# Performance work log

Measured on AMD Instinct MI355X. Metric: run time of the kernel, lower is better.

The kernel has to match this reference:

```python
import jax, jax.numpy as jnp
from jax import lax
import numpy as np

B, EMB, HEADS, LAYERS = 32, 512, 8, 4
SEQ_JD, TOK = 200, 50

def _mask_lg(S):
    # Faithful vectorization of CoKEModel.mask_lg (True = masked)
    m = np.ones((B, HEADS, S, S), dtype=bool)
    rows = np.arange(S)[:, None]
    cols = np.clip(rows - 5 + np.arange(10)[None, :], 0, S - 1)  # window=10, offset -5..4
    for h in range(6):  # local_len = 6 local-window heads
        m[:, h, rows, cols] = False
    m[0, 6:] = False          # global heads unmasked only for batch 0 (faithful to source)
    m[:, :, 0, :] = False     # CLS row attends everywhere
    return m

def _ln_free(x):
    # CoKEModel.layer_norm: no affine, eps=1e-12, rsqrt form
    mu = jnp.mean(x, axis=-1, keepdims=True)
    sx = x - mu
    v = jnp.mean(sx * sx, axis=-1, keepdims=True)
    return sx * jnp.sqrt(1.0 / (v + 1e-12))

def _ln(x, g, b):
    mu = jnp.mean(x, axis=-1, keepdims=True)
    sx = x - mu
    v = jnp.mean(sx * sx, axis=-1, keepdims=True)
    return sx / jnp.sqrt(v + 1e-5) * g + b

def _textcnn(tokens, emb, cws, cbs, fw, fb):
    e = emb[tokens]                        # (N, 50, 1024)
    x = jnp.transpose(e, (0, 2, 1))        # (N, 1024, 50): embed dim as channels
    pooled = []
    for W, b in zip(cws, cbs):             # W: (100, k, 1024)
        rhs = jnp.transpose(W, (0, 2, 1))  # (100, 1024, k)
        y = lax.conv_general_dilated(x, rhs, (1,), 'VALID', dimension_numbers=('NCH', 'OIH', 'NCH'))
        y = jax.nn.relu(y + b[None, :, None])
        pooled.append(jnp.max(y, axis=2))  # global max-pool over time
    return jnp.concatenate(pooled, axis=1) @ fw.T + fb   # (N, 512)

def _encoder(x, mask, wq, bq, wk, bk, wv, bv, wo, bo, l1g, l1b, fw1, fb1, fw2, fb2, l2g, l2b):
    Bb, S, D = x.shape
    dh = D // HEADS
    scale = 1.0 / (dh ** 0.5)
    for l in range(LAYERS):
        q = (x @ wq[l].T + bq[l]).reshape(Bb, S, HEADS, dh)
        k = (x @ wk[l].T + bk[l]).reshape(Bb, S, HEADS, dh)
        v = (x @ wv[l].T + bv[l]).reshape(Bb, S, HEADS, dh)
        s = jnp.einsum('bshd,bthd->bhst', q, k) * scale
        s = jnp.where(mask, -1e9, s)
        a = jax.nn.softmax(s, axis=-1)
        c = jnp.einsum('bhst,bthd->bshd', a, v).reshape(Bb, S, D)
        x = _ln(x + c @ wo[l].T + bo[l], l1g[l], l1b[l])
        h = jax.nn.relu(x @ fw1[l].T + fb1[l])
        x = _ln(x + h @ fw2[l].T + fb2[l], l2g[l], l2b[l])
    return x

def _contrastive(im, s, margin=0.02):
    sc = im @ s.T
    d = jnp.diag(sc)
    cs = jnp.maximum(margin + sc - d[:, None], 0.0)
    ci = jnp.maximum(margin + sc - d[None, :], 0.0)
    eye = jnp.eye(sc.shape[0], dtype=bool)
    cs = jnp.where(eye, 0.0, cs)
    ci = jnp.where(eye, 0.0, ci)
    return jnp.sum(cs) + jnp.sum(ci)

def _forward(floats, src, mask101, mask200):
    (user_info, label_similarity, emb_tc, cw1, cb1, cw2, cb2, cw3, cb3, tfw, tfb,
     wq, bq, wk, bk, wv, bv, wo, bo, l1g, l1b, fw1, fb1, fw2, fb2, l2g, l2b,
     fc1w, fc1b, fc2w, fc2b, fc3w, fc3b, fc4w, fc4b, pscale, pbias) = floats
    cws, cbs = (cw1, cw2, cw3), (cb1, cb2, cb3)
    enc = (wq, bq, wk, bk, wv, bv, wo, bo, l1g, l1b, fw1, fb1, fw2, fb2, l2g, l2b)

    # ---- first pass: first 100 JDs + global CLS token ----
    s1 = _textcnn(src[:, :100].reshape(-1, TOK), emb_tc, cws, cbs, tfw, tfb).reshape(B, 100, EMB)
    s1 = _ln_free(s1)
    s1 = jnp.concatenate([jnp.zeros((B, 1, EMB), s1.dtype), s1], axis=1)  # (B, 101, EMB)
    p = _encoder(s1, mask101, *enc)
    p = jax.nn.gelu(p @ fc1w.T + fc1b, approximate=False)
    p = _ln_free(p)
    p = p * pscale[:, :p.shape[1]] + pbias[:, :p.shape[1]]
    p = p @ fc2w.T + fc2b                      # (B, 101, 204)
    cls_e, tok = p[:, :1], p[:, 1:]
    P = tok @ fc3w.T + fc3b                    # (B, 100, 204)
    clsIII = cls_e @ fc3w.T + fc3b             # (B, 1, 204)
    SLl = jnp.einsum('bsm,bsn->bmn', P, P)     # P^T @ P
    SL_hat = label_similarity[None] + 0.4 * SLl
    outIII = jnp.squeeze(clsIII @ SL_hat, axis=1)  # (B, 204)

    # ---- second pass: all 200 JDs ----
    s2 = _textcnn(src.reshape(-1, TOK), emb_tc, cws, cbs, tfw, tfb).reshape(B, SEQ_JD, EMB)
    s2 = _ln_free(s2)
    ap = _encoder(s2, mask200, *enc)
    ap = jax.nn.gelu(ap @ fc1w.T + fc1b, approximate=False)
    ap = _ln_free(ap)
    ap = ap * pscale[:, :SEQ_JD] + pbias[:, :SEQ_JD]
    p1 = ap @ fc2w.T + fc2b                    # (B, 200, 204)

    nn_ = SEQ_JD // 100  # = 2 neighbors
    eps = 1e-6
    skl_rows, seuc_rows = [], []
    for i in range(nn_):
        # NOTE: faithful to source slicing bug: [i : (i+1)*100]
        c1 = jax.nn.softmax(jnp.mean(p1[:, i:(i + 1) * 100], axis=1), axis=-1)
        a1 = jax.nn.softmax(jnp.mean(ap[:, i:(i + 1) * 100], axis=1), axis=-1)
        rk, re = [], []
        for j in range(nn_):
            c2 = jax.nn.softmax(jnp.mean(p1[:, j:(j + 1) * 100], axis=1), axis=-1)
            a2 = jax.nn.softmax(jnp.mean(ap[:, j:(j + 1) * 100], axis=1), axis=-1)
            rk.append(jnp.sum((c1 + eps) * jnp.log((c1 + eps) / (c2 + eps)), axis=-1))
            re.append(jnp.sqrt(jnp.sum((a1 - a2) ** 2, axis=-1) + 1e-12))
        skl_rows.append(jnp.stack(rk, axis=-1))
        seuc_rows.append(jnp.stack(re, axis=-1))
    skl = jnp.stack(skl_rows, axis=1).reshape(B, -1) * 10.0
    seuc = jnp.stack(seuc_rows, axis=1).reshape(B, -1)
    skl = jax.nn.softmax(skl, axis=-1)
    seuc = jax.nn.softmax(seuc, axis=-1)
    loss_sims = jnp.mean(jnp.sum((skl + eps) * jnp.log((skl + eps) / (seuc + eps)), axis=-1))

    cls4m = jnp.squeeze(cls_e, axis=1)
    user4m = user_info @ fc4w.T + fc4b
    nrm = lambda x: x / jnp.maximum(jnp.linalg.norm(x, axis=1, keepdims=True), 1e-12)
    match = _contrastive(nrm(cls4m), nrm(user4m))

    return (jax.nn.softmax(outIII, axis=-1),
            jax.nn.softmax(cls_e, axis=-1),
            loss_sims * 100000.0,
            match * 0.01)

def setup_inputs():
    key = jax.random.key(0)
    kit = iter(jax.random.split(key, 48))
    def nrm(shape, s=0.02):
        return jax.random.normal(next(kit), shape, jnp.float32) * s
    d = {}
    d['src'] = jax.random.randint(next(kit), (B, SEQ_JD, TOK), 0, 20000)
    d['user_info'] = nrm((B, 142), 1.0)
    d['label_similarity'] = nrm((204, 204))
    d['emb_tc'] = nrm((20000, 1024)).at[0].set(0.0)  # padding_idx=0 row zeroed
    d['cw1'], d['cb1'] = nrm((100, 1, 1024)), jnp.zeros((100,), jnp.float32)
    d['cw2'], d['cb2'] = nrm((100, 2, 1024)), jnp.zeros((100,), jnp.float32)
    d['cw3'], d['cb3'] = nrm((100, 3, 1024)), jnp.zeros((100,), jnp.float32)
    d['tfw'], d['tfb'] = nrm((512, 300)), jnp.zeros((512,), jnp.float32)
    d['wq'], d['bq'] = nrm((LAYERS, EMB, EMB)), jnp.zeros((LAYERS, EMB), jnp.float32)
    d['wk'], d['bk'] = nrm((LAYERS, EMB, EMB)), jnp.zeros((LAYERS, EMB), jnp.float32)
    d['wv'], d['bv'] = nrm((LAYERS, EMB, EMB)), jnp.zeros((LAYERS, EMB), jnp.float32)
    d['wo'], d['bo'] = nrm((LAYERS, EMB, EMB)), jnp.zeros((LAYERS, EMB), jnp.float32)
    d['l1g'], d['l1b'] = jnp.ones((LAYERS, EMB), jnp.float32), jnp.zeros((LAYERS, EMB), jnp.float32)
    d['fw1'], d['fb1'] = nrm((LAYERS, 2048, EMB)), jnp.zeros((LAYERS, 2048), jnp.float32)
    d['fw2'], d['fb2'] = nrm((LAYERS, EMB, 2048)), jnp.zeros((LAYERS, EMB), jnp.float32)
    d['l2g'], d['l2b'] = jnp.ones((LAYERS, EMB), jnp.float32), jnp.zeros((LAYERS, EMB), jnp.float32)
    d['fc1w'], d['fc1b'] = nrm((EMB, EMB)), jnp.zeros((EMB,), jnp.float32)
    d['fc2w'], d['fc2b'] = nrm((204, EMB)), jnp.zeros((204,), jnp.float32)
    d['fc3w'], d['fc3b'] = nrm((204, 204)), jnp.zeros((204,), jnp.float32)
    d['fc4w'], d['fc4b'] = nrm((204, 142)), jnp.zeros((204,), jnp.float32)
    d['pscale'] = jnp.ones((B, 300, EMB), jnp.float32)
    d['pbias'] = jnp.zeros((B, 300, EMB), jnp.float32)
    d['mask101'] = jnp.asarray(_mask_lg(101))
    d['mask200'] = jnp.asarray(_mask_lg(SEQ_JD))
    return d

def reference(src, user_info, label_similarity, emb_tc, cw1, cb1, cw2, cb2, cw3, cb3, tfw, tfb, wq, bq, wk, bk, wv, bv, wo, bo, l1g, l1b, fw1, fb1, fw2, fb2, l2g, l2b, fc1w, fc1b, fc2w, fc2b, fc3w, fc3b, fc4w, fc4b, pscale, pbias, mask101, mask200):
    floats = (user_info, label_similarity, emb_tc, cw1, cb1, cw2, cb2, cw3, cb3, tfw, tfb,
              wq, bq, wk, bk, wv, bv, wo, bo, l1g, l1b, fw1, fb1, fw2, fb2, l2g, l2b,
              fc1w, fc1b, fc2w, fc2b, fc3w, fc3b, fc4w, fc4b, pscale, pbias)
    return _forward(floats, src, mask101, mask200)
```

## Files before the change

kernel.cpp:

```cpp
#include <hip/hip_runtime.h>
#include <math.h>

#define EMB 512
#define HEADS 8
#define NLAYERS 4
#define NB 32
#define SEQ 200
#define TOKN 50
#define DH 64
#define FFND 2048
#define NCLS 204
#define VC 640
#define KD 1024
#define CCH 8
#define CROWS (6400/CCH)
#define CM (CROWS*TOKN)
#define MSEG 16
#define CMT ((CM + 127) / 128)
#define CNT (VC / 128)
#define CT  (CMT * CNT)

typedef __attribute__((ext_vector_type(8))) short v8s;
typedef __attribute__((ext_vector_type(4))) float v4f;
typedef unsigned short ushort_t;
// ... 79 lines not shown
    ll[e] = f2bu(x[e] - hf);
  }
  h.x=hh[0]; h.y=hh[1]; h.z=hh[2]; h.w=hh[3];
  l.x=ll[0]; l.y=ll[1]; l.z=ll[2]; l.w=ll[3];
  *(ushort4*)(hi + i4) = h;
  *(ushort4*)(lo + i4) = l;
}

__global__ void qkvbias_kernel(const float* __restrict__ bq, const float* __restrict__ bk,
                               const float* __restrict__ bv, float* __restrict__ bqkv){
  int l = blockIdx.x;
  for (int j = threadIdx.x; j < 1536; j += 256){
    float v;
    if (j < 512) v = bq[l * 512 + j];
    else if (j < 1024) v = bk[l * 512 + j - 512];
    else v = bv[l * 512 + j - 1024];
    bqkv[l * 1536 + j] = v;
  }
}

__global__ __launch_bounds__(256) void zerobuf_kernel(float* __restrict__ p, size_t n4){
  size_t i = (size_t)blockIdx.x * 256 + threadIdx.x;
  size_t stride = (size_t)gridDim.x * 256;
  for (; i < n4; i += stride)
    ((float4*)p)[i] = make_float4(0.f, 0.f, 0.f, 0.f);
}

__global__ __launch_bounds__(256, 4) void conv_gemm_kernel(
    const int* __restrict__ tok, const ushort_t* __restrict__ embb,
    const ushort_t* __restrict__ Wb, ushort_t* __restrict__ Cout, int Mc)
{
  __shared__ ushort_t Al[128][40];
  __shared__ ushort_t Bl[128][40];
  const int tid = threadIdx.x;
  const int t = xcd_swz(blockIdx.x, CT);
  const int n0 = (t % CNT) * 128;
  const int m0 = (t / CNT) * 128;
  const int wave = tid >> 6, lane = tid & 63;
  const int wm = (wave >> 1) * 64, wn = (wave & 1) * 64;
  const int lcol = lane & 15, lq = lane >> 4;

  v4f acc[4][4];
  #pragma unroll
  for (int i = 0; i < 4; i++)
    #pragma unroll
    for (int j = 0; j < 4; j++) acc[i][j] = (v4f){0.f, 0.f, 0.f, 0.f};

  const int srow = tid >> 1, skh = (tid & 1) * 16;
  const int am = m0 + srow;
  const ushort_t* aep = (am < Mc) ? (embb + (size_t)tok[am] * KD + skh) : nullptr;
  const ushort_t* bep = Wb + (size_t)(n0 + srow) * KD + skh;

  for (int k0 = 0; k0 < KD; k0 += 32){
    uint4 a0 = make_uint4(0,0,0,0), a1 = make_uint4(0,0,0,0);
    if (aep){
      a0 = *(const uint4*)(aep + k0);
      a1 = *(const uint4*)(aep + k0 + 8);
    }
    *(uint4*)&Al[srow][skh]     = a0;
    *(uint4*)&Al[srow][skh + 8] = a1;
    uint4 b0 = *(const uint4*)(bep + k0);
    uint4 b1 = *(const uint4*)(bep + k0 + 8);
    *(uint4*)&Bl[srow][skh]     = b0;
    *(uint4*)&Bl[srow][skh + 8] = b1;
    __syncthreads();

    v8s af[4];
    #pragma unroll
    for (int mi = 0; mi < 4; mi++)
      af[mi] = *(const v8s*)&Al[wm + mi*16 + lcol][lq*8];
    #pragma unroll
    for (int ni = 0; ni < 4; ni++){
      v8s bf = *(const v8s*)&Bl[wn + ni*16 + lcol][lq*8];
      #pragma unroll
      for (int mi = 0; mi < 4; mi++)
        acc[mi][ni] = __builtin_amdgcn_mfma_f32_16x16x32_bf16(af[mi], bf, acc[mi][ni], 0, 0, 0);
    }
    __syncthreads();
  }

  #pragma unroll
  for (int ni = 0; ni < 4; ni++){
    int n = n0 + wn + ni*16 + lcol;
    #pragma unroll
    for (int mi = 0; mi < 4; mi++){
      int mbase = m0 + wm + mi*16 + lq*4;
      #pragma unroll
      for (int rg = 0; rg < 4; rg++){
        int m = mbase + rg;
        if (m < Mc) Cout[(size_t)m * VC + n] = f2bu(acc[mi][ni][rg]);
      }
    }
  }
}

__global__ __launch_bounds__(256, 2) void pool_fc_kernel(
    const ushort_t* __restrict__ Cc, const float* __restrict__ tfwT,
    const float* __restrict__ cb1, const float* __restrict__ cb2,
    const float* __restrict__ cb3, const float* __restrict__ tfb,
    float* __restrict__ basep)
{
  __shared__ ushort_t Sg[VC][54];
  __shared__ float pooled[304];
  __shared__ float red[8];
  const int tid = threadIdx.x;
  const int r = blockIdx.x;

  const unsigned* cr = (const unsigned*)(Cc + (size_t)r * TOKN * VC);
  for (int p = 0; p < TOKN; p++){
    for (int t = tid; t < VC/2; t += 256){
      unsigned u = cr[p * (VC/2) + t];
      Sg[2*t][p]   = (ushort_t)(u & 0xFFFFu);
      Sg[2*t+1][p] = (ushort_t)(u >> 16);
    }
  }
  __syncthreads();

  for (int c = tid; c < 300; c += 256){
    float mv = -1e30f;
    if (c < 100){
      float bb = cb1[c];
      for (int p = 0; p < 50; p++) mv = fmaxf(mv, bu2f(Sg[c][p]) + bb);
    } else if (c < 200){
      int o = c - 100; float bb = cb2[o];
      for (int p = 0; p < 49; p++)
        mv = fmaxf(mv, bu2f(Sg[100 + o][p]) + bu2f(Sg[200 + o][p + 1]) + bb);
    } else {
      int o = c - 200; float bb = cb3[o];
      for (int p = 0; p < 48; p++)
        mv = fmaxf(mv, bu2f(Sg[300 + o][p]) + bu2f(Sg[400 + o][p + 1]) + bu2f(Sg[500 + o][p + 2]) + bb);
    }
    pooled[c] = fmaxf(mv, 0.f);
  }
  __syncthreads();

  float v0 = tfb[tid], v1 = tfb[tid + 256];
  for (int j = 0; j < 300; j++){
    float pj = pooled[j];
    v0 = fmaf(pj, tfwT[(size_t)j * EMB + tid], v0);
    v1 = fmaf(pj, tfwT[(size_t)j * EMB + tid + 256], v1);
  }
  float tot = block_reduce(v0 + v1, red, 4, false);
  float mu = tot * (1.f / 512.f);
  float s0 = v0 - mu, s1 = v1 - mu;
  float var = block_reduce(s0 * s0 + s1 * s1, red, 4, false) * (1.f / 512.f);
  float sc = sqrtf(1.f / (var + 1e-12f));
  basep[(size_t)r * EMB + tid] = s0 * sc;
  basep[(size_t)r * EMB + tid + 256] = s1 * sc;
}

__global__ __launch_bounds__(256, 3) void gemm_mfma_pre_kernel(
    const float* __restrict__ A, const ushort_t* __restrict__ Whi,
    const ushort_t* __restrict__ Wlo, const float* __restrict__ bias,
    float* __restrict__ C, int M, int N, int K, int ldc, int act, int mt, int nt)
{
  __shared__ ushort_t Ahi[128][40];
  __shared__ ushort_t Alo[128][40];
  __shared__ ushort_t Bhi[128][40];
  __shared__ ushort_t Blo[128][40];

  const int tid = threadIdx.x;
  const int t = xcd_swz(blockIdx.x, mt * nt);
  const int n0 = (t % nt) * 128, m0 = (t / nt) * 128;
  const int wave = tid >> 6, lane = tid & 63;
  const int wm = (wave >> 1) * 64, wn = (wave & 1) * 64;
  const int lcol = lane & 15, lq = lane >> 4;

  v4f acc[4][4];
  #pragma unroll
  for (int i = 0; i < 4; i++)
    #pragma unroll
    for (int j = 0; j < 4; j++) acc[i][j] = (v4f){0.f, 0.f, 0.f, 0.f};

  const int srow = tid >> 1;
  const int skh  = (tid & 1) * 16;
  const int am = m0 + srow, bn = n0 + srow;
  const bool mok = (am < M), nok = (bn < N);
  const float* ap = A + (size_t)am * K + skh;
  const ushort_t* bph = Whi + (size_t)bn * K + skh;
  const ushort_t* bpl = Wlo + (size_t)bn * K + skh;

  for (int k0 = 0; k0 < K; k0 += 32){
    bool kfull = (k0 + 32 <= K);
    {
      float av[16];
      if (mok && kfull){
        #pragma unroll
        for (int q = 0; q < 4; q++){
          float4 f = *(const float4*)(ap + k0 + q*4);
          av[q*4+0]=f.x; av[q*4+1]=f.y; av[q*4+2]=f.z; av[q*4+3]=f.w;
        }
      } else {
        #pragma unroll
        for (int e = 0; e < 16; e++){
          int k = k0 + skh + e;
          av[e] = (mok && k < K) ? ap[k0 + e] : 0.f;
        }
      }
      uint4 uh[2], ul[2];
      #pragma unroll
      for (int h = 0; h < 2; h++){
        unsigned hw[8], lw[8];
        #pragma unroll
        for (int e = 0; e < 8; e++){
          float x = av[h*8+e];
          unsigned u = __float_as_uint(x);
          float hf = __uint_as_float(u & 0xFFFF0000u);
          hw[e] = u >> 16;
          lw[e] = f2bu(x - hf);
        }
        uh[h] = make_uint4(hw[0]|(hw[1]<<16), hw[2]|(hw[3]<<16), hw[4]|(hw[5]<<16), hw[6]|(hw[7]<<16));
        ul[h] = make_uint4(lw[0]|(lw[1]<<16), lw[2]|(lw[3]<<16), lw[4]|(lw[5]<<16), lw[6]|(lw[7]<<16));
      }
      *(uint4*)&Ahi[srow][skh]     = uh[0];
      *(uint4*)&Ahi[srow][skh + 8] = uh[1];
      *(uint4*)&Alo[srow][skh]     = ul[0];
      *(uint4*)&Alo[srow][skh + 8] = ul[1];
    }
    {
      uint4 h0 = make_uint4(0,0,0,0), h1 = h0, l0 = h0, l1 = h0;
      if (nok && kfull){
        h0 = *(const uint4*)(bph + k0);
        h1 = *(const uint4*)(bph + k0 + 8);
        l0 = *(const uint4*)(bpl + k0);
        l1 = *(const uint4*)(bpl + k0 + 8);
      } else if (nok){
        ushort_t he[16], le[16];
        #pragma unroll
        for (int e = 0; e < 16; e++){
          int k = k0 + skh + e;
          he[e] = (k < K) ? bph[k0 + e] : (ushort_t)0;
          le[e] = (k < K) ? bpl[k0 + e] : (ushort_t)0;
        }
        h0 = *(uint4*)&he[0]; h1 = *(uint4*)&he[8];
        l0 = *(uint4*)&le[0]; l1 = *(uint4*)&le[8];
      }
      *(uint4*)&Bhi[srow][skh]     = h0;
      *(uint4*)&Bhi[srow][skh + 8] = h1;
      *(uint4*)&Blo[srow][skh]     = l0;
      *(uint4*)&Blo[srow][skh + 8] = l1;
    }
    __syncthreads();

    v8s ah[4], al[4];
    #pragma unroll
    for (int mi = 0; mi < 4; mi++){
      ah[mi] = *(const v8s*)&Ahi[wm + mi*16 + lcol][lq*8];
      al[mi] = *(const v8s*)&Alo[wm + mi*16 + lcol][lq*8];
    }
    #pragma unroll
    for (int ni = 0; ni < 4; ni++){
      v8s bh = *(const v8s*)&Bhi[wn + ni*16 + lcol][lq*8];
      v8s bl = *(const v8s*)&Blo[wn + ni*16 + lcol][lq*8];
      #pragma unroll
      for (int mi = 0; mi < 4; mi++){
        acc[mi][ni] = __builtin_amdgcn_mfma_f32_16x16x32_bf16(ah[mi], bh, acc[mi][ni], 0, 0, 0);
        acc[mi][ni] = __builtin_amdgcn_mfma_f32_16x16x32_bf16(al[mi], bh, acc[mi][ni], 0, 0, 0);
        acc[mi][ni] = __builtin_amdgcn_mfma_f32_16x16x32_bf16(ah[mi], bl, acc[mi][ni], 0, 0, 0);
      }
    }
    __syncthreads();
  }

  #pragma unroll
  for (int ni = 0; ni < 4; ni++){
    int n = n0 + wn + ni*16 + lcol;
    if (n >= N) continue;
    float bv = bias[n];
    #pragma unroll
    for (int mi = 0; mi < 4; mi++){
      int mbase = m0 + wm + mi*16 + lq*4;
      #pragma unroll
      for (int rg = 0; rg < 4; rg++){
        int m = mbase + rg;
        if (m >= M) continue;
        float v = acc[mi][ni][rg] + bv;
        if (act == 1) v = fmaxf(v, 0.f);
        else if (act == 2) v = 0.5f * v * (1.f + erff(v * 0.70710678118654752f));
        C[(size_t)m * ldc + n] = v;
      }
    }
  }
}

__global__ __launch_bounds__(256, 4) void gemm_mfma_pre64_kernel(
    const float* __restrict__ A, const ushort_t* __restrict__ Whi,
    const ushort_t* __restrict__ Wlo, const float* __restrict__ bias,
    float* __restrict__ C, int M, int N, int K, int ldc, int act, int mt, int nt, int ks)
{
  __shared__ ushort_t Ahi[128][40];
  __shared__ ushort_t Alo[128][40];
  __shared__ ushort_t Bhi[64][40];
  __shared__ ushort_t Blo[64][40];

  const int tid = threadIdx.x;
  const int tiles = mt * nt;
  const int t_ = xcd_swz(blockIdx.x, tiles * ks);
  const int slice = t_ / tiles;
  const int t = t_ % tiles;
  const int n0 = (t % nt) * 64, m0 = (t / nt) * 128;
  const int kstep = ((K + 31) / 32 + ks - 1) / ks;
  const int kb = slice * kstep * 32;
  const int ke = min(K, kb + kstep * 32);
  if (kb >= ke) return;
  const int wave = tid >> 6, lane = tid & 63;
  const int wm = (wave >> 1) * 64, wn = (wave & 1) * 32;
  const int lcol = lane & 15, lq = lane >> 4;

  v4f acc[4][2];
  #pragma unroll
  for (int i = 0; i < 4; i++)
    #pragma unroll
    for (int j = 0; j < 2; j++) acc[i][j] = (v4f){0.f, 0.f, 0.f, 0.f};

  const int srow = tid >> 1;
  const int skh  = (tid & 1) * 16;
  const int am = m0 + srow;
  const bool mok = (am < M);
  const float* ap = A + (size_t)am * K + skh;
  const int brow = tid >> 2;
  const int bkq  = (tid & 3) * 8;
  const int bn = n0 + brow;
  const bool nok = (bn < N);
  const ushort_t* bph = Whi + (size_t)bn * K + bkq;
  const ushort_t* bpl = Wlo + (size_t)bn * K + bkq;

  for (int k0 = kb; k0 < ke; k0 += 32){
    bool kfull = (k0 + 32 <= K);
    {
      float av[16];
      if (mok && kfull){
        #pragma unroll
        for (int q = 0; q < 4; q++){
          float4 f = *(const float4*)(ap + k0 + q*4);
          av[q*4+0]=f.x; av[q*4+1]=f.y; av[q*4+2]=f.z; av[q*4+3]=f.w;
        }
      } else {
        #pragma unroll
        for (int e = 0; e < 16; e++){
          int k = k0 + skh + e;
          av[e] = (mok && k < K) ? ap[k0 + e] : 0.f;
        }
      }
      uint4 uh[2], ul[2];
      #pragma unroll
      for (int h = 0; h < 2; h++){
        unsigned hw[8], lw[8];
        #pragma unroll
        for (int e = 0; e < 8; e++){
          float x = av[h*8+e];
          unsigned u = __float_as_uint(x);
          float hf = __uint_as_float(u & 0xFFFF0000u);
          hw[e] = u >> 16;
          lw[e] = f2bu(x - hf);
        }
        uh[h] = make_uint4(hw[0]|(hw[1]<<16), hw[2]|(hw[3]<<16), hw[4]|(hw[5]<<16), hw[6]|(hw[7]<<16));
        ul[h] = make_uint4(lw[0]|(lw[1]<<16), lw[2]|(lw[3]<<16), lw[4]|(lw[5]<<16), lw[6]|(lw[7]<<16));
      }
      *(uint4*)&Ahi[srow][skh]     = uh[0];
      *(uint4*)&Ahi[srow][skh + 8] = uh[1];
      *(uint4*)&Alo[srow][skh]     = ul[0];
      *(uint4*)&Alo[srow][skh + 8] = ul[1];
    }
    {
      uint4 h0 = make_uint4(0,0,0,0), l0 = h0;
      if (nok && kfull){
        h0 = *(const uint4*)(bph + k0);
        l0 = *(const uint4*)(bpl + k0);
      } else if (nok){
        ushort_t he[8], le[8];
        #pragma unroll
        for (int e = 0; e < 8; e++){
          int k = k0 + bkq + e;
          he[e] = (k < K) ? bph[k0 + e] : (ushort_t)0;
          le[e] = (k < K) ? bpl[k0 + e] : (ushort_t)0;
        }
        h0 = *(uint4*)&he[0];
        l0 = *(uint4*)&le[0];
      }
      *(uint4*)&Bhi[brow][bkq] = h0;
      *(uint4*)&Blo[brow][bkq] = l0;
    }
    __syncthreads();

    v8s ah[4], al[4];
    #pragma unroll
    for (int mi = 0; mi < 4; mi++){
      ah[mi] = *(const v8s*)&Ahi[wm + mi*16 + lcol][lq*8];
      al[mi] = *(const v8s*)&Alo[wm + mi*16 + lcol][lq*8];
    }
    #pragma unroll
    for (int ni = 0; ni < 2; ni++){
      v8s bh = *(const v8s*)&Bhi[wn + ni*16 + lcol][lq*8];
      v8s bl = *(const v8s*)&Blo[wn + ni*16 + lcol][lq*8];
      #pragma unroll
      for (int mi = 0; mi < 4; mi++){
        acc[mi][ni] = __builtin_amdgcn_mfma_f32_16x16x32_bf16(ah[mi], bh, acc[mi][ni], 0, 0, 0);
        acc[mi][ni] = __builtin_amdgcn_mfma_f32_16x16x32_bf16(al[mi], bh, acc[mi][ni], 0, 0, 0);
        acc[mi][ni] = __builtin_amdgcn_mfma_f32_16x16x32_bf16(ah[mi], bl, acc[mi][ni], 0, 0, 0);
      }
    }
    __syncthreads();
  }

  #pragma unroll
  for (int ni = 0; ni < 2; ni++){
    int n = n0 + wn + ni*16 + lcol;
    if (n >= N) continue;
    float bv = (ks == 1 || slice == 0) ? bias[n] : 0.f;
    #pragma unroll
    for (int mi = 0; mi < 4; mi++){
      int mbase = m0 + wm + mi*16 + lq*4;
      #pragma unroll
      for (int rg = 0; rg < 4; rg++){
        int m = mbase + rg;
        if (m >= M) continue;
        float v = acc[mi][ni][rg] + bv;
        if (ks == 1){
          if (act == 1) v = fmaxf(v, 0.f);
          else if (act == 2) v = 0.5f * v * (1.f + erff(v * 0.70710678118654752f));
          C[(size_t)m * ldc + n] = v;
        } else {
          atomicAdd(&C[(size_t)m * ldc + n], v);
        }
      }
    }
  }
}

__global__ __launch_bounds__(256, 2) void gemm_mfma_kernel(
    const float* __restrict__ A, const float* __restrict__ W,
    const float* __restrict__ bias, float* __restrict__ C,
// ... 444 lines not shown
    const float* __restrict__ p1, const float* __restrict__ ap,
    float* __restrict__ part)
{
  const int blk = blockIdx.x;
  const int bi = blk / MSEG, seg = blk % MSEG;
  const int b = bi >> 1, i = bi & 1;
  const int start = i;
  const int cnt = (i == 0) ? 100 : 199;
  const int per = (cnt + MSEG - 1) / MSEG;
  const int r0 = seg * per;
  const int r1 = min(r0 + per, cnt);
  float* dst = part + (size_t)blk * 720;
  for (int c = threadIdx.x; c < NCLS + EMB; c += 256){
    float s = 0.f;
    if (c < NCLS){
      for (int rr = r0; rr < r1; rr++)
        s += p1[((size_t)(b * SEQ + start + rr)) * NCLS + c];
    } else {
      int cc = c - NCLS;
      for (int rr = r0; rr < r1; rr++)
        s += ap[((size_t)(b * SEQ + start + rr)) * EMB + cc];
    }
    dst[c] = s;
  }
}

__global__ __launch_bounds__(256) void means_final_kernel(
    const float* __restrict__ part, float* __restrict__ mp, float* __restrict__ ma)
{
  const int bi = blockIdx.x;
  const int i = bi & 1;
  const float icnt = (i == 0) ? (1.f / 100.f) : (1.f / 199.f);
  for (int c = threadIdx.x; c < NCLS + EMB; c += 256){
    float s = 0.f;
    #pragma unroll
    for (int g = 0; g < MSEG; g++)
      s += part[((size_t)(bi * MSEG + g)) * 720 + c];
    if (c < NCLS) mp[(size_t)bi * NCLS + c] = s * icnt;
    else          ma[(size_t)bi * EMB + (c - NCLS)] = s * icnt;
  }
}

__global__ __launch_bounds__(64) void klfinal_kernel(
    const float* __restrict__ cbuf, const float* __restrict__ abuf, float* __restrict__ acc)
{
  const int b = blockIdx.x, lane = threadIdx.x;
  float rk[4], re[4];
  #pragma unroll
  for (int pr = 0; pr < 4; pr++){
    int i = pr >> 1, j = pr & 1;
    const float* c1 = cbuf + ((size_t)(b * 2 + i)) * NCLS;
    const float* c2 = cbuf + ((size_t)(b * 2 + j)) * NCLS;
    float s = 0.f;
    for (int n = lane; n < NCLS; n += 64){
      float x = c1[n] + 1e-6f, y = c2[n] + 1e-6f;
      s += x * logf(x / y);
    }
    #pragma unroll
    for (int o = 32; o > 0; o >>= 1) s += __shfl_down(s, o, 64);
    rk[pr] = __shfl(s, 0, 64);
    const float* a1 = abuf + ((size_t)(b * 2 + i)) * EMB;
    const float* a2 = abuf + ((size_t)(b * 2 + j)) * EMB;
    float s2 = 0.f;
    for (int n = lane; n < EMB; n += 64){
      float dd = a1[n] - a2[n];
      s2 += dd * dd;
    }
    #pragma unroll
    for (int o = 32; o > 0; o >>= 1) s2 += __shfl_down(s2, o, 64);
    re[pr] = sqrtf(__shfl(s2, 0, 64) + 1e-12f);
  }
  if (lane == 0){
    float sk[4], se[4];
    float mk = -INFINITY, me = -INFINITY;
    for (int p = 0; p < 4; p++){
      sk[p] = rk[p] * 10.f;
      mk = fmaxf(mk, sk[p]);
      se[p] = re[p];
      me = fmaxf(me, se[p]);
    }
    float ssk = 0.f, sse = 0.f;
    for (int p = 0; p < 4; p++){ sk[p] = expf(sk[p] - mk); ssk += sk[p]; se[p] = expf(se[p] - me); sse += se[p]; }
    float loss = 0.f;
    for (int p = 0; p < 4; p++){
      float x = sk[p] / ssk + 1e-6f, y = se[p] / sse + 1e-6f;
      loss += x * logf(x / y);
    }
    atomicAdd(acc, loss);
  }
}

__global__ void finalize_kernel(const float* __restrict__ acc, float* __restrict__ out){
  if (threadIdx.x == 0) out[13056] = acc[0] * (100000.f / 32.f);
}

extern "C" void kernel_launch(void* const* d_in, const int* in_sizes, int n_in,
                              void* d_out, int out_size, void* d_ws, size_t ws_size,
                              hipStream_t stream)
{
  (void)in_sizes; (void)n_in; (void)out_size;
  const int*   src  = (const int*)  d_in[0];
  const float* user_info = (const float*)d_in[1];
  const float* ls   = (const float*)d_in[2];
  const float* emb  = (const float*)d_in[3];
  const float* cw1  = (const float*)d_in[4];  const float* cb1 = (const float*)d_in[5];
  const float* cw2  = (const float*)d_in[6];  const float* cb2 = (const float*)d_in[7];
  const float* cw3  = (const float*)d_in[8];  const float* cb3 = (const float*)d_in[9];
  const float* tfw  = (const float*)d_in[10]; const float* tfb = (const float*)d_in[11];
  const float* wq   = (const float*)d_in[12]; const float* bq  = (const float*)d_in[13];
  const float* wk   = (const float*)d_in[14]; const float* bk  = (const float*)d_in[15];
  const float* wv   = (const float*)d_in[16]; const float* bv  = (const float*)d_in[17];
  const float* wo   = (const float*)d_in[18]; const float* bo  = (const float*)d_in[19];
  const float* l1g  = (const float*)d_in[20]; const float* l1b = (const float*)d_in[21];
  const float* fw1  = (const float*)d_in[22]; const float* fb1 = (const float*)d_in[23];
  const float* fw2  = (const float*)d_in[24]; const float* fb2 = (const float*)d_in[25];
  const float* l2g  = (const float*)d_in[26]; const float* l2b = (const float*)d_in[27];
  const float* fc1w = (const float*)d_in[28]; const float* fc1b= (const float*)d_in[29];
  const float* fc2w = (const float*)d_in[30]; const float* fc2b= (const float*)d_in[31];
  const float* fc3w = (const float*)d_in[32]; const float* fc3b= (const float*)d_in[33];
  const float* fc4w = (const float*)d_in[34]; const float* fc4b= (const float*)d_in[35];
  const float* pscale = (const float*)d_in[36];
  const float* pbias  = (const float*)d_in[37];
  float* out = (float*)d_out;
  float* ws = (float*)d_ws;

  size_t off = 0;
  auto alloc = [&](size_t n){ float* p = ws + off; off += ((n + 3) & ~(size_t)3); return p; };
  float* base = alloc(6400ULL * EMB);
  float* x1   = alloc((size_t)NB * 101 * EMB);
  float* qkv  = alloc(6400ULL * 1536);
  float* ctx  = alloc(6400ULL * EMB);
  float* proj = alloc(6400ULL * EMB);
  float* hb   = alloc(6400ULL * FFND);
  float* p2   = alloc(6400ULL * NCLS);
  float* clsE = alloc((size_t)NB * NCLS);
  float* tok  = alloc(3200ULL * NCLS);
  float* Pb   = alloc(3200ULL * NCLS);
  float* cls3 = alloc((size_t)NB * NCLS);
  float* SLh  = alloc((size_t)NB * NCLS * NCLS);
  float* o3   = alloc((size_t)NB * NCLS);
  float* u4   = alloc((size_t)NB * NCLS);
  float* imn  = alloc((size_t)NB * NCLS);
  float* sn   = alloc((size_t)NB * NCLS);
  float* mp   = alloc(64ULL * NCLS);
  float* ma   = alloc(64ULL * EMB);
  float* cbf  = alloc(64ULL * NCLS);
  float* abf  = alloc(64ULL * EMB);
  float* lacc = alloc(4);
  float* vmb  = alloc((size_t)NB * HEADS * DH);
  ushort_t* Wb = (ushort_t*)alloc((size_t)VC * KD / 2);
  float* tfwT = alloc(300ULL * EMB);
  float* bqkv = alloc(4ULL * 1536);
  ushort_t* embb = (ushort_t*)qkv;
  const size_t OQKV = 0, OWO = 3145728, OF1 = 4194304, OF2 = 8388608;
  const size_t OC1 = 12582912, OC2 = 12845056, OC3 = 12949504, WTOT = 12991120;
  ushort_t* WhiA = (ushort_t*)alloc((WTOT + 1) / 2);
  ushort_t* WloA = (ushort_t*)alloc((WTOT + 1) / 2);
  const bool presplit = (off * sizeof(float) <= ws_size);

  auto gemm_f32 = [&](const float* A, const float* W, const float* bi, float* C,
                      int M, int N, int K, int act){
    dim3 g((N + 63) / 64, (M + 63) / 64);
    gemm_kernel<<<g, 256, 0, stream>>>(A, W, bi, C, M, N, K, act);
  };
  auto gemm_fly = [&](const float* A, const float* W, const float* bi, float* C,
                      int M, int N, int K, int ldc, int act){
    dim3 g((N + 127) / 128, (M + 127) / 128);
    gemm_mfma_kernel<<<g, 256, 0, stream>>>(A, W, bi, C, M, N, K, ldc, act);
  };
  auto gemm_pre = [&](const float* A, size_t woff, const float* bi, float* C,
                      int M, int N, int K, int ldc, int act){
    int mt = (M + 127) / 128;
    if (N <= 512){
      int nt = (N + 63) / 64;
      int tiles = mt * nt;
      int ks = 1;
      if (act == 0 && K >= 1024){
        while (ks < 8 && tiles * ks * 2 <= 2048 && K / (ks * 2) >= 128) ks *= 2;
      }
      if (ks > 1){
        size_t n4 = ((size_t)M * N) / 4;
        int zg = (int)min((n4 + 255) / 256, (size_t)2048);
        zerobuf_kernel<<<zg, 256, 0, stream>>>(C, n4);
      }
      gemm_mfma_pre64_kernel<<<tiles * ks, 256, 0, stream>>>(
          A, WhiA + woff, WloA + woff, bi, C, M, N, K, ldc, act, mt, nt, ks);
    } else {
      int nt = (N + 127) / 128;
      gemm_mfma_pre_kernel<<<mt * nt, 256, 0, stream>>>(
          A, WhiA + woff, WloA + woff, bi, C, M, N, K, ldc, act, mt, nt);
    }
  };
  auto split = [&](const float* srcw, size_t woff, int n){
    split_kernel<<<(n / 4 + 255) / 256, 256, 0, stream>>>(srcw, WhiA + woff, WloA + woff, n);
  };

  prep_w_kernel<<<(VC * KD / 4 + 255) / 256, 256, 0, stream>>>(cw1, cw2, cw3, Wb);
  prep_embbf_kernel<<<(int)((20000ULL * KD / 4 + 255) / 256), 256, 0, stream>>>(emb, embb);
  prep_tfwT_kernel<<<(300 * EMB + 255) / 256, 256, 0, stream>>>(tfw, tfwT);
  if (presplit){
    for (int l = 0; l < NLAYERS; l++){
      split(wq + (size_t)l * 262144, OQKV + (size_t)l * 786432,          262144);
      split(wk + (size_t)l * 262144, OQKV + (size_t)l * 786432 + 262144, 262144);
      split(wv + (size_t)l * 262144, OQKV + (size_t)l * 786432 + 524288, 262144);
      split(wo + (size_t)l * 262144, OWO + (size_t)l * 262144, 262144);
      split(fw1 + (size_t)l * 1048576, OF1 + (size_t)l * 1048576, 1048576);
      split(fw2 + (size_t)l * 1048576, OF2 + (size_t)l * 1048576, 1048576);
    }
    split(fc1w, OC1, 262144);
    split(fc2w, OC2, NCLS * EMB);
    split(fc3w, OC3, NCLS * NCLS);
    qkvbias_kernel<<<4, 256, 0, stream>>>(bq, bk, bv, bqkv);
  }

  for (int c = 0; c < CCH; c++){
    conv_gemm_kernel<<<CT, 256, 0, stream>>>(
        src + (size_t)c * CM, embb, Wb, (ushort_t*)hb, CM);
    pool_fc_kernel<<<CROWS, 256, 0, stream>>>(
        (ushort_t*)hb, tfwT, cb1, cb2, cb3, tfb, base + (size_t)c * CROWS * EMB);
  }
  buildx1_kernel<<<(NB * 101 * EMB + 255) / 256, 256, 0, stream>>>(base, x1);

  auto encoder = [&](float* x, int S){
    int M = NB * S;
    for (int l = 0; l < NLAYERS; l++){
      if (presplit){
        gemm_pre(x, OQKV + (size_t)l * 786432, bqkv + l * 1536, qkv, M, 1536, EMB, 1536, 0);
      } else {
        gemm_fly(x, wq + (size_t)l * EMB * EMB, bq + l * EMB, qkv,        M, EMB, EMB, 1536, 0);
        gemm_fly(x, wk + (size_t)l * EMB * EMB, bk + l * EMB, qkv + 512,  M, EMB, EMB, 1536, 0);
        gemm_fly(x, wv + (size_t)l * EMB * EMB, bv + l * EMB, qkv + 1024, M, EMB, EMB, 1536, 0);
      }
      vmean_kernel<<<NB * HEADS, 64, 0, stream>>>(qkv, vmb, S);
      attn_full_kernel<<<NB * HEADS + 2 * (S - 1), 64, 0, stream>>>(qkv, ctx, S);
      attn_band_kernel<<<(NB * 6 * (S - 1) + 3) / 4, 256, 0, stream>>>(qkv, ctx, S);
      vmfill_kernel<<<((NB - 1) * 2 * (S - 1) * 64 + 255) / 256, 256, 0, stream>>>(vmb, ctx, S);
      if (presplit) gemm_pre(ctx, OWO + (size_t)l * 262144, bo + l * EMB, proj, M, EMB, EMB, EMB, 0);
      else gemm_fly(ctx, wo + (size_t)l * EMB * EMB, bo + l * EMB, proj, M, EMB, EMB, EMB, 0);
      ln_kernel<<<M, 256, 0, stream>>>(proj, x, l1g + l * EMB, l1b + l * EMB, nullptr, nullptr, x, S, 1e-5f);
      if (presplit) gemm_pre(x, OF1 + (size_t)l * 1048576, fb1 + l * FFND, hb, M, FFND, EMB, FFND, 1);
      else gemm_fly(x, fw1 + (size_t)l * FFND * EMB, fb1 + l * FFND, hb, M, FFND, EMB, FFND, 1);
      if (presplit) gemm_pre(hb, OF2 + (size_t)l * 1048576, fb2 + l * EMB, proj, M, EMB, FFND, EMB, 0);
      else gemm_fly(hb, fw2 + (size_t)l * EMB * FFND, fb2 + l * EMB, proj, M, EMB, FFND, EMB, 0);
      ln_kernel<<<M, 256, 0, stream>>>(proj, x, l2g + l * EMB, l2b + l * EMB, nullptr, nullptr, x, S, 1e-5f);
    }
    if (presplit) gemm_pre(x, OC1, fc1b, ctx, M, EMB, EMB, EMB, 2);
    else gemm_fly(x, fc1w, fc1b, ctx, M, EMB, EMB, EMB, 2);
    ln_kernel<<<M, 256, 0, stream>>>(ctx, nullptr, nullptr, nullptr, pscale, pbias, ctx, S, 1e-12f);
    if (presplit) gemm_pre(ctx, OC2, fc2b, p2, M, NCLS, EMB, NCLS, 0);
    else gemm_fly(ctx, fc2w, fc2b, p2, M, NCLS, EMB, NCLS, 0);
  };

  encoder(x1, 101);
  extract_kernel<<<(NB * 101 * NCLS + 255) / 256, 256, 0, stream>>>(p2, clsE, tok);
  if (presplit) gemm_pre(tok, OC3, fc3b, Pb, 3200, NCLS, NCLS, NCLS, 0);
  else gemm_fly(tok, fc3w, fc3b, Pb, 3200, NCLS, NCLS, NCLS, 0);
  gemm_f32(clsE, fc3w, fc3b, cls3, NB, NCLS, NCLS, 0);
  slhat_kernel<<<NB * NCLS, 256, 0, stream>>>(Pb, ls, SLh);
  outIII_kernel<<<NB, 256, 0, stream>>>(cls3, SLh, o3);
  softmax_out_kernel<<<NB, 256, 0, stream>>>(o3, out, NCLS);
  softmax_out_kernel<<<NB, 256, 0, stream>>>(clsE, out + NB * NCLS, NCLS);
  gemm_f32(user_info, fc4w, fc4b, u4, NB, NCLS, 142, 0);
  normalize_kernel<<<64, 256, 0, stream>>>(clsE, u4, imn, sn);
  contrastive_kernel<<<1, 1024, 0, stream>>>(imn, sn, out);

  encoder(base, SEQ);
  zero_kernel<<<1, 64, 0, stream>>>(lacc);
  means_part_kernel<<<64 * MSEG, 256, 0, stream>>>(p2, ctx, hb);
  means_final_kernel<<<64, 256, 0, stream>>>(hb, mp, ma);
  softmax_out_kernel<<<64, 256, 0, stream>>>(mp, cbf, NCLS);
  softmax_out_kernel<<<64, 256, 0, stream>>>(ma, abf, EMB);
  klfinal_kernel<<<NB, 64, 0, stream>>>(cbf, abf, lacc);
  finalize_kernel<<<1, 64, 0, stream>>>(lacc, out);
}
```

Measured before the change: 4.968 ms.

## Emit pre-split bf16 hi/lo FFN activations from FFN1 epilogue for FFN2

The FFN1 GEMM epilogue now writes the ReLU output directly as bf16 hi and lo halves instead of fp32. A new split-K GEMM variant reads those pre-split A operands straight into shared memory, with no per-tile fp32-to-bf16 split. This saves the conversion work in FFN2's A loads and keeps the intermediate the same size, since two ushort arrays replace one float array. It adds a second GEMM kernel variant, and the lo half goes through the f2bu rounding helper.

Result: no change. 4.949 ms (-0.4%).

```diff
diff --git a/kernel.cpp b/kernel.cpp
--- a/kernel.cpp
+++ b/kernel.cpp
@@ -255,7 +255,8 @@
 __global__ __launch_bounds__(256, 3) void gemm_mfma_pre_kernel(
     const float* __restrict__ A, const ushort_t* __restrict__ Whi,
     const ushort_t* __restrict__ Wlo, const float* __restrict__ bias,
-    float* __restrict__ C, int M, int N, int K, int ldc, int act, int mt, int nt)
+    float* __restrict__ C, int M, int N, int K, int ldc, int act, int mt, int nt,
+    ushort_t* __restrict__ Chi, ushort_t* __restrict__ Clo, int splitout)
 {
   __shared__ ushort_t Ahi[128][40];
   __shared__ ushort_t Alo[128][40];
@@ -380,7 +381,144 @@
         float v = acc[mi][ni][rg] + bv;
         if (act == 1) v = fmaxf(v, 0.f);
         else if (act == 2) v = 0.5f * v * (1.f + erff(v * 0.70710678118654752f));
-        C[(size_t)m * ldc + n] = v;
+        if (splitout){
+          unsigned u = __float_as_uint(v);
+          float hf = __uint_as_float(u & 0xFFFF0000u);
+          Chi[(size_t)m * ldc + n] = (ushort_t)(u >> 16);
+          Clo[(size_t)m * ldc + n] = f2bu(v - hf);
+        } else {
+          C[(size_t)m * ldc + n] = v;
+        }
+      }
+    }
+  }
+}
+
+__global__ __launch_bounds__(256, 4) void gemm_mfma_pre64A_kernel(
+    const ushort_t* __restrict__ Ahig, const ushort_t* __restrict__ Alog,
+    const ushort_t* __restrict__ Whi, const ushort_t* __restrict__ Wlo,
+    const float* __restrict__ bias, float* __restrict__ C,
+    int M, int N, int K, int ldc, int mt, int nt, int ks)
+{
+  __shared__ ushort_t Ahi[128][40];
+  __shared__ ushort_t Alo[128][40];
+  __shared__ ushort_t Bhi[64][40];
+  __shared__ ushort_t Blo[64][40];
+
+  const int tid = threadIdx.x;
+  const int tiles = mt * nt;
+  const int t_ = xcd_swz(blockIdx.x, tiles * ks);
+  const int slice = t_ / tiles;
+  const int t = t_ % tiles;
+  const int n0 = (t % nt) * 64, m0 = (t / nt) * 128;
+  const int kstep = ((K + 31) / 32 + ks - 1) / ks;
+  const int kb = slice * kstep * 32;
+  const int ke = min(K, kb + kstep * 32);
+  if (kb >= ke) return;
+  const int wave = tid >> 6, lane = tid & 63;
+  const int wm = (wave >> 1) * 64, wn = (wave & 1) * 32;
+  const int lcol = lane & 15, lq = lane >> 4;
+
+  v4f acc[4][2];
+  #pragma unroll
+  for (int i = 0; i < 4; i++)
+    #pragma unroll
+    for (int j = 0; j < 2; j++) acc[i][j] = (v4f){0.f, 0.f, 0.f, 0.f};
+
+  const int srow = tid >> 1;
+  const int skh  = (tid & 1) * 16;
+  const int am = m0 + srow;
+  const bool mok = (am < M);
+  const ushort_t* aph = Ahig + (size_t)am * K + skh;
+  const ushort_t* apl = Alog + (size_t)am * K + skh;
+  const int brow = tid >> 2;
+  const int bkq  = (tid & 3) * 8;
+  const int bn = n0 + brow;
+  const bool nok = (bn < N);
+  const ushort_t* bph = Whi + (size_t)bn * K + bkq;
+  const ushort_t* bpl = Wlo + (size_t)bn * K + bkq;
+
+  for (int k0 = kb; k0 < ke; k0 += 32){
+    bool kfull = (k0 + 32 <= K);
+    {
+      uint4 h0 = make_uint4(0,0,0,0), h1 = h0, l0 = h0, l1 = h0;
+      if (mok && kfull){
+        h0 = *(const uint4*)(aph + k0);
+        h1 = *(const uint4*)(aph + k0 + 8);
+        l0 = *(const uint4*)(apl + k0);
+        l1 = *(const uint4*)(apl + k0 + 8);
+      } else if (mok){
+        ushort_t he[16], le[16];
+        #pragma unroll
+        for (int e = 0; e < 16; e++){
+          int k = k0 + skh + e;
+          he[e] = (k < K) ? aph[k0 + e] : (ushort_t)0;
+          le[e] = (k < K) ? apl[k0 + e] : (ushort_t)0;
+        }
+        h0 = *(uint4*)&he[0]; h1 = *(uint4*)&he[8];
+        l0 = *(uint4*)&le[0]; l1 = *(uint4*)&le[8];
+      }
+      *(uint4*)&Ahi[srow][skh]     = h0;
+      *(uint4*)&Ahi[srow][skh + 8] = h1;
+      *(uint4*)&Alo[srow][skh]     = l0;
+      *(uint4*)&Alo[srow][skh + 8] = l1;
+    }
+    {
+      uint4 h0 = make_uint4(0,0,0,0), l0 = h0;
+      if (nok && kfull){
+        h0 = *(const uint4*)(bph + k0);
+        l0 = *(const uint4*)(bpl + k0);
+      } else if (nok){
+        ushort_t he[8], le[8];
+        #pragma unroll
+        for (int e = 0; e < 8; e++){
+          int k = k0 + bkq + e;
+          he[e] = (k < K) ? bph[k0 + e] : (ushort_t)0;
+          le[e] = (k < K) ? bpl[k0 + e] : (ushort_t)0;
+        }
+        h0 = *(uint4*)&he[0];
+        l0 = *(uint4*)&le[0];
+      }
+      *(uint4*)&Bhi[brow][bkq] = h0;
+      *(uint4*)&Blo[brow][bkq] = l0;
+    }
+    __syncthreads();
+
+    v8s ah[4], al[4];
+    #pragma unroll
+    for (int mi = 0; mi < 4; mi++){
+      ah[mi] = *(const v8s*)&Ahi[wm + mi*16 + lcol][lq*8];
+      al[mi] = *(const v8s*)&Alo[wm + mi*16 + lcol][lq*8];
+    }
+    #pragma unroll
+    for (int ni = 0; ni < 2; ni++){
+      v8s bh = *(const v8s*)&Bhi[wn + ni*16 + lcol][lq*8];
+      v8s bl = *(const v8s*)&Blo[wn + ni*16 + lcol][lq*8];
+      #pragma unroll
+      for (int mi = 0; mi < 4; mi++){
+        acc[mi][ni] = __builtin_amdgcn_mfma_f32_16x16x32_bf16(ah[mi], bh, acc[mi][ni], 0, 0, 0);
+        acc[mi][ni] = __builtin_amdgcn_mfma_f32_16x16x32_bf16(al[mi], bh, acc[mi][ni], 0, 0, 0);
+        acc[mi][ni] = __builtin_amdgcn_mfma_f32_16x16x32_bf16(ah[mi], bl, acc[mi][ni], 0, 0, 0);
+      }
+    }
+    __syncthreads();
+  }
+
+  #pragma unroll
+  for (int ni = 0; ni < 2; ni++){
+    int n = n0 + wn + ni*16 + lcol;
+    if (n >= N) continue;
+    float bv = (ks == 1 || slice == 0) ? bias[n] : 0.f;
+    #pragma unroll
+    for (int mi = 0; mi < 4; mi++){
+      int mbase = m0 + wm + mi*16 + lq*4;
+      #pragma unroll
+      for (int rg = 0; rg < 4; rg++){
+        int m = mbase + rg;
+        if (m >= M) continue;
+        float v = acc[mi][ni][rg] + bv;
+        if (ks == 1) C[(size_t)m * ldc + n] = v;
+        else atomicAdd(&C[(size_t)m * ldc + n], v);
       }
     }
   }
@@ -1131,6 +1269,8 @@
   float* tfwT = alloc(300ULL * EMB);
   float* bqkv = alloc(4ULL * 1536);
   ushort_t* embb = (ushort_t*)qkv;
+  ushort_t* hbh = (ushort_t*)hb;
+  ushort_t* hbl = hbh + 6400ULL * FFND;
   const size_t OQKV = 0, OWO = 3145728, OF1 = 4194304, OF2 = 8388608;
   const size_t OC1 = 12582912, OC2 = 12845056, OC3 = 12949504, WTOT = 12991120;
   ushort_t* WhiA = (ushort_t*)alloc((WTOT + 1) / 2);
@@ -1167,7 +1307,8 @@
     } else {
       int nt = (N + 127) / 128;
       gemm_mfma_pre_kernel<<<mt * nt, 256, 0, stream>>>(
-          A, WhiA + woff, WloA + woff, bi, C, M, N, K, ldc, act, mt, nt);
+          A, WhiA + woff, WloA + woff, bi, C, M, N, K, ldc, act, mt, nt,
+          nullptr, nullptr, 0);
     }
   };
   auto split = [&](const float* srcw, size_t woff, int n){
@@ -1217,10 +1358,27 @@
       if (presplit) gemm_pre(ctx, OWO + (size_t)l * 262144, bo + l * EMB, proj, M, EMB, EMB, EMB, 0);
       else gemm_fly(ctx, wo + (size_t)l * EMB * EMB, bo + l * EMB, proj, M, EMB, EMB, EMB, 0);
       ln_kernel<<<M, 256, 0, stream>>>(proj, x, l1g + l * EMB, l1b + l * EMB, nullptr, nullptr, x, S, 1e-5f);
-      if (presplit) gemm_pre(x, OF1 + (size_t)l * 1048576, fb1 + l * FFND, hb, M, FFND, EMB, FFND, 1);
-      else gemm_fly(x, fw1 + (size_t)l * FFND * EMB, fb1 + l * FFND, hb, M, FFND, EMB, FFND, 1);
-      if (presplit) gemm_pre(hb, OF2 + (size_t)l * 1048576, fb2 + l * EMB, proj, M, EMB, FFND, EMB, 0);
-      else gemm_fly(hb, fw2 + (size_t)l * EMB * FFND, fb2 + l * EMB, proj, M, EMB, FFND, EMB, 0);
+      if (presplit){
+        int mt = (M + 127) / 128, nt2 = FFND / 128;
+        gemm_mfma_pre_kernel<<<mt * nt2, 256, 0, stream>>>(
+            x, WhiA + OF1 + (size_t)l * 1048576, WloA + OF1 + (size_t)l * 1048576,
+            fb1 + l * FFND, nullptr, M, FFND, EMB, FFND, 1, mt, nt2, hbh, hbl, 1);
+        int mt2 = (M + 127) / 128, nt3 = EMB / 64;
+        int tiles = mt2 * nt3;
+        int ks = 1;
+        while (ks < 8 && tiles * ks * 2 <= 2048 && FFND / (ks * 2) >= 128) ks *= 2;
+        if (ks > 1){
+          size_t n4 = ((size_t)M * EMB) / 4;
+          int zg = (int)min((n4 + 255) / 256, (size_t)2048);
+          zerobuf_kernel<<<zg, 256, 0, stream>>>(proj, n4);
+        }
+        gemm_mfma_pre64A_kernel<<<tiles * ks, 256, 0, stream>>>(
+            hbh, hbl, WhiA + OF2 + (size_t)l * 1048576, WloA + OF2 + (size_t)l * 1048576,
+            fb2 + l * EMB, proj, M, EMB, FFND, EMB, mt2, nt3, ks);
+      } else {
+        gemm_fly(x, fw1 + (size_t)l * FFND * EMB, fb1 + l * FFND, hb, M, FFND, EMB, FFND, 1);
+        gemm_fly(hb, fw2 + (size_t)l * EMB * FFND, fb2 + l * EMB, proj, M, EMB, FFND, EMB, 0);
+      }
       ln_kernel<<<M, 256, 0, stream>>>(proj, x, l2g + l * EMB, l2b + l * EMB, nullptr, nullptr, x, S, 1e-5f);
     }
     if (presplit) gemm_pre(x, OC1, fc1b, ctx, M, EMB, EMB, EMB, 2);
```
